# Kernel tuning notes

Measured on AMD Instinct MI355X. Metric: run time of the kernel, lower is better.

Reference implementation:

```python
import jax, jax.numpy as jnp
import numpy as np
from math import sqrt
from itertools import product

NUM_CLASSES = 21
TOP_K = 200
VAR = (0.1, 0.2)
CONF_THRESH = 0.01
NMS_THRESH = 0.45
EPS = 1e-6
BATCH = 32


def make_priors():
    # Exact SSD300 PriorBox generation (8732 boxes, cx/cy/w/h in [0,1])
    image_size = 300
    feature_maps = [38, 19, 10, 5, 3, 1]
    steps = [8, 16, 32, 64, 100, 300]
    min_sizes = [30, 60, 111, 162, 213, 264]
    max_sizes = [60, 111, 162, 213, 264, 315]
    ars = [[2], [2, 3], [2, 3], [2, 3], [2], [2]]
    mean = []
    for k, f in enumerate(feature_maps):
        for i, j in product(range(f), repeat=2):
            f_k = image_size / steps[k]
            cx = (j + 0.5) / f_k
            cy = (i + 0.5) / f_k
            s_k = min_sizes[k] / image_size
            mean += [cx, cy, s_k, s_k]
            s_kp = sqrt(s_k * (max_sizes[k] / image_size))
            mean += [cx, cy, s_kp, s_kp]
            for ar in ars[k]:
                mean += [cx, cy, s_k * sqrt(ar), s_k / sqrt(ar)]
                mean += [cx, cy, s_k / sqrt(ar), s_k * sqrt(ar)]
    pri = np.asarray(mean, np.float32).reshape(-1, 4)
    return np.clip(pri, 0.0, 1.0)


def setup_inputs() -> dict:
    key = jax.random.key(0)
    k1, k2 = jax.random.split(key)
    priors = jnp.asarray(make_priors())  # [8732, 4]
    P = priors.shape[0]
    loc = jax.random.normal(k1, (BATCH, P, 4), jnp.float32) * 0.5
    conf = jax.random.normal(k2, (BATCH, P, NUM_CLASSES), jnp.float32)
    return {"loc": loc, "conf": conf, "priors": priors}


def _decode(loc, priors):
    # calc_predicted_bboxes: cx/cy offset + clamped log-w/h, then corner clamp [0,1]
    pri = jnp.clip(priors, EPS, None)
    cx = pri[:, 0] + loc[:, 0] * VAR[0] * pri[:, 2]
    cy = pri[:, 1] + loc[:, 1] * VAR[0] * pri[:, 3]
    lw = jnp.clip(loc[:, 2] * VAR[1], -4.0, 4.0)
    lh = jnp.clip(loc[:, 3] * VAR[1], -4.0, 4.0)
    w = pri[:, 2] * jnp.exp(lw)
    h = pri[:, 3] * jnp.exp(lh)
    return jnp.stack([
        jnp.clip(cx - w / 2, 0.0, 1.0), jnp.clip(cy - h / 2, 0.0, 1.0),
        jnp.clip(cx + w / 2, 0.0, 1.0), jnp.clip(cy + h / 2, 0.0, 1.0)], axis=1)


def _iou_matrix(b):  # b: [K,4] -> [K,K]
    area = (b[:, 2] - b[:, 0]) * (b[:, 3] - b[:, 1])
    lt = jnp.maximum(b[:, None, :2], b[None, :, :2])
    rb = jnp.minimum(b[:, None, 2:], b[None, :, 2:])
    wh = jnp.clip(rb - lt, 0.0)
    inter = wh[..., 0] * wh[..., 1]
    union = area[:, None] + area[None, :] - inter
    return inter / jnp.maximum(union, 1e-12)


def _per_class(boxes, scores):
    # boxes [P,4], scores [P] -> [TOP_K, 5] rows of [score, x1, y1, x2, y2]
    valid = (scores > CONF_THRESH) \
        & (boxes[:, 2] > boxes[:, 0] + EPS) & (boxes[:, 3] > boxes[:, 1] + EPS)
    masked = jnp.where(valid, scores, -1.0)
    top_s, top_i = jax.lax.top_k(masked, TOP_K)  # highest-score candidates
    top_b = boxes[top_i]
    top_valid = top_s > CONF_THRESH  # invalid padded entries have score -1
    ious = _iou_matrix(top_b)
    pos = jnp.arange(TOP_K)

    def body(i, alive):
        keep_i = alive[i] & top_valid[i]
        suppress = keep_i & (ious[i] > NMS_THRESH) & (pos > i)
        return alive & ~suppress

    alive = jax.lax.fori_loop(0, TOP_K, body, jnp.ones(TOP_K, bool))
    keep = alive & top_valid
    # compact kept detections to the front, preserving score order
    order = jnp.argsort(jnp.where(keep, pos, TOP_K + pos))
    rows = jnp.concatenate([top_s[:, None], top_b], axis=1)[order]
    return jnp.where(keep[order][:, None], rows, 0.0)


def reference(loc, conf, priors):
    probs = jax.nn.softmax(jnp.clip(conf, -100.0, 100.0), axis=-1)  # [B,P,C]
    boxes = jax.vmap(_decode, in_axes=(0, None))(loc, priors)       # [B,P,4]

    def per_image(b, p):
        fg = jax.vmap(_per_class, in_axes=(None, 1))(b, p[:, 1:])   # [C-1,K,5]
        return jnp.concatenate([jnp.zeros((1, TOP_K, 5), b.dtype), fg], axis=0)

    return jax.vmap(per_image)(boxes, probs)  # [B, C, K, 5]
```

## Files before the change

kernel.cpp:

```cpp
#include <hip/hip_runtime.h>
#include <cstdint>

#define P_BOX 8732
#define NBOX_TOTAL 279424
#define BATCH 32
#define NCLS 21
#define NFG 20
#define TOPK 200
#define NTH 256
#define NCH 9
#define CAND_CAP 512
#define NBKT 2048
#define NORM 0xBC23D70Bu
#define LIM (1u << 26)
#define CONF_F4 1466976

typedef unsigned long long u64;

__device__ __forceinline__ uint32_t score_key(float m) {
  uint32_t b = __float_as_uint(m);
  return (b & 0x80000000u) ? ~b : (b | 0x80000000u);
}
__device__ __forceinline__ float key_score(uint32_t k) {
  uint32_t b = (k & 0x80000000u) ? (k ^ 0x80000000u) : ~k;
  return __uint_as_float(b);
}

__device__ __forceinline__ float4 decode_box(const float4 pr, const float4 lc) {
  float px = fmaxf(pr.x, 1e-6f), py = fmaxf(pr.y, 1e-6f);
  float pw = fmaxf(pr.z, 1e-6f), ph = fmaxf(pr.w, 1e-6f);
  float cx = px + lc.x * 0.1f * pw;
  float cy = py + lc.y * 0.1f * ph;
  float lw = fminf(fmaxf(lc.z * 0.2f, -4.0f), 4.0f);
  float lh = fminf(fmaxf(lc.w * 0.2f, -4.0f), 4.0f);
  float w = pw * expf(lw);
  float h = ph * expf(lh);
  float4 r;
  r.x = fminf(fmaxf(cx - 0.5f * w, 0.0f), 1.0f);
  r.y = fminf(fmaxf(cy - 0.5f * h, 0.0f), 1.0f);
  r.z = fminf(fmaxf(cx + 0.5f * w, 0.0f), 1.0f);
  r.w = fminf(fmaxf(cy + 0.5f * h, 0.0f), 1.0f);
  return r;
}

__global__ __launch_bounds__(256) void prep_kernel(
    const float* __restrict__ loc, const float* __restrict__ conf,
    const float* __restrict__ priors, uint32_t* __restrict__ keys) {
  __shared__ float s_conf[256 * 21];
  const int t = threadIdx.x;
  const int blk = blockIdx.x;
  const float4* cf4 = (const float4*)conf;
  size_t base4 = (size_t)blk * 1344;
#pragma unroll
  for (int i = t; i < 1344; i += 256) {
    size_t g4 = base4 + i;
    if (g4 < CONF_F4) ((float4*)s_conf)[i] = cf4[g4];
  }
  __syncthreads();
  int g = blk * 256 + t;
  if (g >= NBOX_TOTAL) return;
  int b = g / P_BOX, p = g - b * P_BOX;
  float x[NCLS];
  float mx = -1e30f;
#pragma unroll
  for (int i = 0; i < NCLS; ++i) {
    float v = fminf(fmaxf(s_conf[t * 21 + i], -100.0f), 100.0f);
    x[i] = v;
    mx = fmaxf(mx, v);
  }
  float s = 0.0f;
#pragma unroll
  for (int i = 0; i < NCLS; ++i) {
    x[i] = expf(x[i] - mx);
    s += x[i];
  }
  float4 bx = decode_box(((const float4*)priors)[p], ((const float4*)loc)[g]);
  bool bok = (bx.z > bx.x + 1e-6f) && (bx.w > bx.y + 1e-6f);
#pragma unroll
  for (int ci = 1; ci < NCLS; ++ci) {
    float sc = x[ci] / s;
    float m = (bok && sc > 0.01f) ? sc : -1.0f;
    keys[((size_t)(b * NFG) + (ci - 1)) * P_BOX + p] = score_key(m) - NORM;
  }
}

__device__ __forceinline__ int cnt_ge(const uint32_t* kv, uint32_t X) {
  int n = 0;
#pragma unroll
  for (int j = 0; j < NCH * 4; ++j) n += (kv[j] >= X && kv[j] < LIM) ? 1 : 0;
  return n;
}
__device__ __forceinline__ int cnt_eq_idx(const uint32_t* kv, int t, uint32_t T, uint32_t I) {
  int n = 0;
#pragma unroll
  for (int ch = 0; ch < NCH; ++ch) {
#pragma unroll
    for (int e = 0; e < 4; ++e) {
      int p = ch * 1024 + t * 4 + e;
      n += (kv[ch * 4 + e] == T && (uint32_t)(P_BOX - p) >= I) ? 1 : 0;
    }
  }
  return n;
}

__device__ __forceinline__ int block_count(int v, int t, int* s_cnt, int& it) {
#pragma unroll
  for (int o = 32; o > 0; o >>= 1) v += __shfl_down(v, o, 64);
  int slot = it % 3;
  if (t == 0) s_cnt[(it + 1) % 3] = 0;
  if ((t & 63) == 0) atomicAdd(&s_cnt[slot], v);
  __syncthreads();
  int r = s_cnt[slot];
  ++it;
  return r;
}

__device__ __forceinline__ int3 select_bucket(const int* s_hist, int* s_S,
                                              int* s_wt, int* s_res, int need,
                                              int t) {
  const int BPT = NBKT / NTH;
  int base = t * BPT;
  int ps = 0;
#pragma unroll
  for (int i = 0; i < BPT; ++i) ps += s_hist[base + i];
  int l = t & 63, w = t >> 6;
  int v = ps;
#pragma unroll
  for (int off = 1; off < 64; off <<= 1) {
    int o = __shfl_down(v, off, 64);
    v += (l + off < 64) ? o : 0;
  }
  if (l == 0) s_wt[w] = v;
  __syncthreads();
  int hi = 0;
#pragma unroll
  for (int w2 = 0; w2 < NTH / 64; ++w2) hi += (w2 > w) ? s_wt[w2] : 0;
  int S = v + hi;
  s_S[t] = S;
  __syncthreads();
  if (t == 0 && s_S[0] < need) {
    s_res[0] = 0; s_res[1] = s_S[0]; s_res[2] = 0;
  } else if (s_S[t] >= need && (t == NTH - 1 || s_S[t + 1] < need)) {
    int suf = (t == NTH - 1) ? 0 : s_S[t + 1];
    int B = base, M = 0;
    for (int j = base + BPT - 1; j >= base; --j) {
      suf += s_hist[j];
      if (suf >= need) { B = j; M = suf; break; }
    }
    s_res[0] = B; s_res[1] = M; s_res[2] = M - s_hist[B];
  }
  __syncthreads();
  return make_int3(s_res[0], s_res[1], s_res[2]);
}

template <bool USE_WS>
__global__ __launch_bounds__(256) void task_kernel(
    const float* __restrict__ loc, const float* __restrict__ conf,
    const float* __restrict__ priors, const uint32_t* __restrict__ keys,
    float* __restrict__ out) {
  const int t = threadIdx.x;
  const int task = blockIdx.x;
  const int b = task / NCLS, c = task - b * NCLS;
  float* ob = out + (size_t)task * TOPK * 5;

  if (c == 0) {
    float4 z = make_float4(0.f, 0.f, 0.f, 0.f);
    for (int i = t; i < TOPK * 5 / 4; i += NTH) ((float4*)ob)[i] = z;
    return;
  }
  const int ft = b * NFG + (c - 1);

  __shared__ alignas(16) int s_hist[NBKT];
  __shared__ alignas(16) u64 s_cand[CAND_CAP];
  __shared__ u64 s_sel[TOPK];
  __shared__ float4 s_box[TOPK];
  __shared__ float s_area[TOPK];
  __shared__ float s_score[TOPK];
  __shared__ u64 s_nxt[2][4];
  __shared__ short s_kept[TOPK];
  __shared__ int s_wt[NTH / 64];
  __shared__ int s_res[3];
  __shared__ int s_cnt[3];
  __shared__ int s_m;
  int* s_S = (int*)s_cand;
  float* s_out = (float*)s_hist;

  if (t == 0) { s_cnt[0] = 0; s_cnt[1] = 0; s_cnt[2] = 0; s_m = 0; }
  for (int i = t; i < NBKT; i += NTH) s_hist[i] = 0;

  uint32_t kv[NCH * 4];
  if (USE_WS) {
    const uint4* kp = (const uint4*)(keys + (size_t)ft * P_BOX);
#pragma unroll
    for (int ch = 0; ch < 8; ++ch) {
      uint4 v = kp[ch * 256 + t];
      kv[ch * 4 + 0] = v.x; kv[ch * 4 + 1] = v.y;
      kv[ch * 4 + 2] = v.z; kv[ch * 4 + 3] = v.w;
    }
    if (t < 135) {
      uint4 v = kp[2048 + t];
      kv[32] = v.x; kv[33] = v.y; kv[34] = v.z; kv[35] = v.w;
    } else {
      kv[32] = LIM; kv[33] = LIM; kv[34] = LIM; kv[35] = LIM;
    }
  } else {
    for (int ch = 0; ch < NCH; ++ch) {
      int p0 = ch * 1024 + 4 * t;
#pragma unroll
      for (int e = 0; e < 4; ++e) {
        int p = p0 + e;
        uint32_t k = LIM;
        if (p < P_BOX) {
          const float* cf = conf + (size_t)(b * P_BOX + p) * NCLS;
          float x[NCLS];
          float mx = -1e30f;
#pragma unroll
          for (int i = 0; i < NCLS; ++i) {
            float v = fminf(fmaxf(cf[i], -100.0f), 100.0f);
            x[i] = v;
            mx = fmaxf(mx, v);
          }
          float ssum = 0.0f, ec = 0.0f;
#pragma unroll
          for (int i = 0; i < NCLS; ++i) {
            float ex = expf(x[i] - mx);
            ssum += ex;
            if (i == c) ec = ex;
          }
          float sc = ec / ssum;
          float4 bx = decode_box(((const float4*)priors)[p],
                                 ((const float4*)loc)[(size_t)b * P_BOX + p]);
          bool valid = (sc > 0.01f) && (bx.z > bx.x + 1e-6f) && (bx.w > bx.y + 1e-6f);
          k = score_key(valid ? sc : -1.0f) - NORM;
        }
        kv[ch * 4 + e] = k;
      }
    }
  }
  __syncthreads();

#pragma unroll
  for (int j = 0; j < NCH * 4; ++j)
    if (kv[j] < LIM) atomicAdd(&s_hist[kv[j] >> 15], 1);
  __syncthreads();
  int3 r1 = select_bucket(s_hist, s_S, s_wt, s_res, TOPK, t);
  uint32_t Tp = (uint32_t)r1.x << 15;
  int M = r1.y;
  bool ex = false;
  uint32_t Tex = 0, I = 0;

  if (M > CAND_CAP) {
    uint32_t B1 = (uint32_t)r1.x;
    int above1 = r1.z;
    __syncthreads();
    for (int i = t; i < NBKT; i += NTH) s_hist[i] = 0;
    __syncthreads();
#pragma unroll
    for (int j = 0; j < NCH * 4; ++j)
      if (kv[j] < LIM && (kv[j] >> 15) == B1)
        atomicAdd(&s_hist[(kv[j] >> 4) & (NBKT - 1)], 1);
    __syncthreads();
    int3 r2 = select_bucket(s_hist, s_S, s_wt, s_res, TOPK - above1, t);
    Tp = (B1 << 15) + ((uint32_t)r2.x << 4);
    M = above1 + r2.y;
    if (M > CAND_CAP) {
      int it = 0;
      uint32_t lo = Tp, hi = LIM;
      while (hi - lo > 1) {
        uint32_t mid = lo + ((hi - lo) >> 1);
        int cnt = block_count(cnt_ge(kv, mid), t, s_cnt, it);
        if (cnt >= TOPK) lo = mid; else hi = mid;
      }
      Tex = lo;
      int G = block_count(cnt_ge(kv, Tex + 1), t, s_cnt, it);
      int R = TOPK - G;
      uint32_t lo2 = 1, hi2 = P_BOX + 1;
      while (hi2 - lo2 > 1) {
        uint32_t mid = lo2 + ((hi2 - lo2) >> 1);
        int cnt = block_count(cnt_eq_idx(kv, t, Tex, mid), t, s_cnt, it);
        if (cnt >= R) lo2 = mid; else hi2 = mid;
      }
      I = lo2;
      ex = true;
    }
  }
  __syncthreads();

  {
    const int lane = t & 63;
#pragma unroll
    for (int ch = 0; ch < NCH; ++ch) {
#pragma unroll
      for (int e = 0; e < 4; ++e) {
        uint32_t k = kv[ch * 4 + e];
        int p = ch * 1024 + 4 * t + e;
        bool take = (k < LIM) &&
                    (ex ? (k > Tex || (k == Tex && (uint32_t)(P_BOX - p) >= I))
                        : (k >= Tp));
        u64 m = __ballot(take);
        if (m) {
          int leader = __ffsll((long long)m) - 1;
          int base = 0;
          if (lane == leader) base = atomicAdd(&s_m, __popcll(m));
          base = __shfl(base, leader, 64);
          if (take) {
            int pre = __popcll(m & ((1ull << lane) - 1ull));
            int ix = base + pre;
            if (ix < CAND_CAP)
              s_cand[ix] = ((u64)k << 32) | (uint32_t)(P_BOX - p);
          }
        }
      }
    }
  }
  __syncthreads();
  M = min(s_m, CAND_CAP);
  int nsel = min(M, TOPK);

  for (int ci = t; ci < M; ci += NTH) {
    u64 mine = s_cand[ci];
    int r = 0;
    int j = 0;
    for (; j + 8 <= M; j += 8) {
      u64 a0 = s_cand[j + 0], a1 = s_cand[j + 1], a2 = s_cand[j + 2],
          a3 = s_cand[j + 3], a4 = s_cand[j + 4], a5 = s_cand[j + 5],
          a6 = s_cand[j + 6], a7 = s_cand[j + 7];
      r += (a0 > mine) + (a1 > mine) + (a2 > mine) + (a3 > mine) +
           (a4 > mine) + (a5 > mine) + (a6 > mine) + (a7 > mine);
    }
    for (; j < M; ++j) r += (s_cand[j] > mine) ? 1 : 0;
    if (r < TOPK) s_sel[r] = mine;
  }
  __syncthreads();

  if (t < TOPK) {
    if (t < nsel) {
      u64 w = s_sel[t];
      uint32_t k = (uint32_t)(w >> 32);
      int p = P_BOX - (int)(uint32_t)(w & 0xFFFFFFFFull);
      float4 bx = decode_box(((const float4*)priors)[p],
                             ((const float4*)loc)[(size_t)b * P_BOX + p]);
      s_box[t] = bx;
      s_area[t] = (bx.z - bx.x) * (bx.w - bx.y);
      s_score[t] = key_score(k + NORM);
    } else {
      s_box[t] = make_float4(0.f, 0.f, 0.f, 0.f);
      s_area[t] = 0.f;
      s_score[t] = 0.f;
    }
  }
  __syncthreads();

  float4 bj = make_float4(0.f, 0.f, 0.f, 0.f);
  float aj = 0.f;
  const bool validj = (t < nsel);
  if (validj) { bj = s_box[t]; aj = s_area[t]; }
  const int wv = t >> 6;
  u64 cm0 = 0, cm1 = 0, cm2 = 0, cm3 = 0;
#pragma unroll
  for (int band = 0; band < 4; ++band) {
    if (band > wv) break;
    const int base = band * 64;
    const int iend = min(base + 64, nsel);
    u64 w = 0;
#pragma unroll 4
    for (int i = base; i < iend; ++i) {
      float4 bi = s_box[i];
      float ai = s_area[i];
      float lx = fmaxf(bi.x, bj.x), ly = fmaxf(bi.y, bj.y);
      float rx = fminf(bi.z, bj.z), ry = fminf(bi.w, bj.w);
      float iw = fmaxf(rx - lx, 0.0f), ih = fmaxf(ry - ly, 0.0f);
      float inter = iw * ih;
      float uni = ai + aj - inter;
      float iou = inter / fmaxf(uni, 1e-12f);
      bool sup = (i < t) && validj && (iou > 0.45f);
      w |= ((u64)sup) << (i - base);
    }
    if (band == 0) cm0 = w; else if (band == 1) cm1 = w;
    else if (band == 2) cm2 = w; else cm3 = w;
  }

  int q0 = nsel, q1 = nsel - 64, q2 = nsel - 128, q3 = nsel - 192;
  u64 a0 = q0 >= 64 ? ~0ull : (q0 <= 0 ? 0ull : ((1ull << q0) - 1));
  u64 a1 = q1 >= 64 ? ~0ull : (q1 <= 0 ? 0ull : ((1ull << q1) - 1));
  u64 a2 = q2 >= 64 ? ~0ull : (q2 <= 0 ? 0ull : ((1ull << q2) - 1));
  u64 a3 = q3 >= 64 ? ~0ull : (q3 <= 0 ? 0ull : ((1ull << q3) - 1));
  for (int it2 = 0; it2 <= TOPK; ++it2) {
    bool sup = ((cm0 & a0) | (cm1 & a1) | (cm2 & a2) | (cm3 & a3)) != 0ull;
    bool na = validj && !sup;
    u64 m = __ballot(na);
    int buf = it2 & 1;
    if ((t & 63) == 0) s_nxt[buf][t >> 6] = m;
    __syncthreads();
    u64 n0 = s_nxt[buf][0], n1 = s_nxt[buf][1];
    u64 n2 = s_nxt[buf][2], n3 = s_nxt[buf][3];
    bool chg = (n0 != a0) || (n1 != a1) || (n2 != a2) || (n3 != a3);
    a0 = n0; a1 = n1; a2 = n2; a3 = n3;
    if (!chg) break;
  }

  int pc0 = __popcll(a0), pc01 = pc0 + __popcll(a1), pc012 = pc01 + __popcll(a2);
  int nk = pc012 + __popcll(a3);
  if (t < nsel) {
    int word = t >> 6, bit = t & 63;
    u64 wt = (word == 0) ? a0 : (word == 1) ? a1 : (word == 2) ? a2 : a3;
    if ((wt >> bit) & 1ull) {
      int base = (word == 0) ? 0 : (word == 1) ? pc0 : (word == 2) ? pc01 : pc012;
      int r = base + __popcll(wt & ((1ull << bit) - 1ull));
      s_kept[r] = (short)t;
    }
  }
  __syncthreads();

  if (t < TOPK) {
    float o0 = 0.f, o1 = 0.f, o2 = 0.f, o3 = 0.f, o4 = 0.f;
    if (t < nk) {
      int j = s_kept[t];
      o0 = s_score[j];
      float4 bx = s_box[j];
      o1 = bx.x; o2 = bx.y; o3 = bx.z; o4 = bx.w;
    }
    s_out[t * 5 + 0] = o0; s_out[t * 5 + 1] = o1; s_out[t * 5 + 2] = o2;
    s_out[t * 5 + 3] = o3; s_out[t * 5 + 4] = o4;
  }
  __syncthreads();
  for (int i = t; i < TOPK * 5 / 4; i += NTH)
    ((float4*)ob)[i] = ((float4*)s_out)[i];
}

extern "C" void kernel_launch(void* const* d_in, const int* in_sizes, int n_in,
                              void* d_out, int out_size, void* d_ws, size_t ws_size,
                              hipStream_t stream) {
  (void)in_sizes;
  (void)n_in;
  (void)out_size;
  const float* loc = (const float*)d_in[0];
  const float* conf = (const float*)d_in[1];
  const float* priors = (const float*)d_in[2];
  float* out = (float*)d_out;

  size_t keys_bytes = (size_t)BATCH * NFG * P_BOX * sizeof(uint32_t);
  if (ws_size >= keys_bytes) {
    uint32_t* keys = (uint32_t*)d_ws;
    int nprep = (NBOX_TOTAL + 255) / 256;
    prep_kernel<<<nprep, 256, 0, stream>>>(loc, conf, priors, keys);
    task_kernel<true><<<BATCH * NCLS, NTH, 0, stream>>>(loc, conf, priors, keys, out);
  } else {
    task_kernel<false><<<BATCH * NCLS, NTH, 0, stream>>>(loc, conf, priors, nullptr, out);
  }
}
```

Baseline: 133.2 us.

## Drop separate prep kernel and compute class scores inside each task block

Removes the prep kernel that computed softmax and box validity once per box and wrote per-class keys to workspace. Each (image, class) block now recomputes the full softmax and box decode for every prior itself. This saves a kernel launch and the write and read-back of the keys buffer. In exchange it repeats the softmax about 20 times and reads conf with strided, uncoalesced loads from every block.

Result: slower. 417.7 us (+213.5%).

```diff
diff --git a/kernel.cpp b/kernel.cpp
--- a/kernel.cpp
+++ b/kernel.cpp
@@ -2,10 +2,8 @@
 #include <cstdint>
 
 #define P_BOX 8732
-#define NBOX_TOTAL 279424
 #define BATCH 32
 #define NCLS 21
-#define NFG 20
 #define TOPK 200
 #define NTH 256
 #define NCH 9
@@ -13,7 +11,6 @@
 #define NBKT 2048
 #define NORM 0xBC23D70Bu
 #define LIM (1u << 26)
-#define CONF_F4 1466976
 
 typedef unsigned long long u64;
 
@@ -43,47 +40,6 @@
   return r;
 }
 
-__global__ __launch_bounds__(256) void prep_kernel(
-    const float* __restrict__ loc, const float* __restrict__ conf,
-    const float* __restrict__ priors, uint32_t* __restrict__ keys) {
-  __shared__ float s_conf[256 * 21];
-  const int t = threadIdx.x;
-  const int blk = blockIdx.x;
-  const float4* cf4 = (const float4*)conf;
-  size_t base4 = (size_t)blk * 1344;
-#pragma unroll
-  for (int i = t; i < 1344; i += 256) {
-    size_t g4 = base4 + i;
-    if (g4 < CONF_F4) ((float4*)s_conf)[i] = cf4[g4];
-  }
-  __syncthreads();
-  int g = blk * 256 + t;
-  if (g >= NBOX_TOTAL) return;
-  int b = g / P_BOX, p = g - b * P_BOX;
-  float x[NCLS];
-  float mx = -1e30f;
-#pragma unroll
-  for (int i = 0; i < NCLS; ++i) {
-    float v = fminf(fmaxf(s_conf[t * 21 + i], -100.0f), 100.0f);
-    x[i] = v;
-    mx = fmaxf(mx, v);
-  }
-  float s = 0.0f;
-#pragma unroll
-  for (int i = 0; i < NCLS; ++i) {
-    x[i] = expf(x[i] - mx);
-    s += x[i];
-  }
-  float4 bx = decode_box(((const float4*)priors)[p], ((const float4*)loc)[g]);
-  bool bok = (bx.z > bx.x + 1e-6f) && (bx.w > bx.y + 1e-6f);
-#pragma unroll
-  for (int ci = 1; ci < NCLS; ++ci) {
-    float sc = x[ci] / s;
-    float m = (bok && sc > 0.01f) ? sc : -1.0f;
-    keys[((size_t)(b * NFG) + (ci - 1)) * P_BOX + p] = score_key(m) - NORM;
-  }
-}
-
 __device__ __forceinline__ int cnt_ge(const uint32_t* kv, uint32_t X) {
   int n = 0;
 #pragma unroll
@@ -153,11 +109,9 @@
   return make_int3(s_res[0], s_res[1], s_res[2]);
 }
 
-template <bool USE_WS>
 __global__ __launch_bounds__(256) void task_kernel(
     const float* __restrict__ loc, const float* __restrict__ conf,
-    const float* __restrict__ priors, const uint32_t* __restrict__ keys,
-    float* __restrict__ out) {
+    const float* __restrict__ priors, float* __restrict__ out) {
   const int t = threadIdx.x;
   const int task = blockIdx.x;
   const int b = task / NCLS, c = task - b * NCLS;
@@ -168,7 +122,6 @@
     for (int i = t; i < TOPK * 5 / 4; i += NTH) ((float4*)ob)[i] = z;
     return;
   }
-  const int ft = b * NFG + (c - 1);
 
   __shared__ alignas(16) int s_hist[NBKT];
   __shared__ alignas(16) u64 s_cand[CAND_CAP];
@@ -189,52 +142,36 @@
   for (int i = t; i < NBKT; i += NTH) s_hist[i] = 0;
 
   uint32_t kv[NCH * 4];
-  if (USE_WS) {
-    const uint4* kp = (const uint4*)(keys + (size_t)ft * P_BOX);
-#pragma unroll
-    for (int ch = 0; ch < 8; ++ch) {
-      uint4 v = kp[ch * 256 + t];
-      kv[ch * 4 + 0] = v.x; kv[ch * 4 + 1] = v.y;
-      kv[ch * 4 + 2] = v.z; kv[ch * 4 + 3] = v.w;
-    }
-    if (t < 135) {
-      uint4 v = kp[2048 + t];
-      kv[32] = v.x; kv[33] = v.y; kv[34] = v.z; kv[35] = v.w;
-    } else {
-      kv[32] = LIM; kv[33] = LIM; kv[34] = LIM; kv[35] = LIM;
-    }
-  } else {
-    for (int ch = 0; ch < NCH; ++ch) {
-      int p0 = ch * 1024 + 4 * t;
-#pragma unroll
-      for (int e = 0; e < 4; ++e) {
-        int p = p0 + e;
-        uint32_t k = LIM;
-        if (p < P_BOX) {
-          const float* cf = conf + (size_t)(b * P_BOX + p) * NCLS;
-          float x[NCLS];
-          float mx = -1e30f;
-#pragma unroll
-          for (int i = 0; i < NCLS; ++i) {
-            float v = fminf(fmaxf(cf[i], -100.0f), 100.0f);
-            x[i] = v;
-            mx = fmaxf(mx, v);
-          }
-          float ssum = 0.0f, ec = 0.0f;
-#pragma unroll
-          for (int i = 0; i < NCLS; ++i) {
-            float ex = expf(x[i] - mx);
-            ssum += ex;
-            if (i == c) ec = ex;
-          }
-          float sc = ec / ssum;
-          float4 bx = decode_box(((const float4*)priors)[p],
-                                 ((const float4*)loc)[(size_t)b * P_BOX + p]);
-          bool valid = (sc > 0.01f) && (bx.z > bx.x + 1e-6f) && (bx.w > bx.y + 1e-6f);
-          k = score_key(valid ? sc : -1.0f) - NORM;
+  for (int ch = 0; ch < NCH; ++ch) {
+    int p0 = ch * 1024 + 4 * t;
+#pragma unroll
+    for (int e = 0; e < 4; ++e) {
+      int p = p0 + e;
+      uint32_t k = LIM;
+      if (p < P_BOX) {
+        const float* cf = conf + (size_t)(b * P_BOX + p) * NCLS;
+        float x[NCLS];
+        float mx = -1e30f;
+#pragma unroll
+        for (int i = 0; i < NCLS; ++i) {
+          float v = fminf(fmaxf(cf[i], -100.0f), 100.0f);
+          x[i] = v;
+          mx = fmaxf(mx, v);
         }
-        kv[ch * 4 + e] = k;
+        float ssum = 0.0f, ec = 0.0f;
+#pragma unroll
+        for (int i = 0; i < NCLS; ++i) {
+          float ex = expf(x[i] - mx);
+          ssum += ex;
+          if (i == c) ec = ex;
+        }
+        float sc = ec / ssum;
+        float4 bx = decode_box(((const float4*)priors)[p],
+                               ((const float4*)loc)[(size_t)b * P_BOX + p]);
+        bool valid = (sc > 0.01f) && (bx.z > bx.x + 1e-6f) && (bx.w > bx.y + 1e-6f);
+        k = score_key(valid ? sc : -1.0f) - NORM;
       }
+      kv[ch * 4 + e] = k;
     }
   }
   __syncthreads();
@@ -434,18 +371,12 @@
   (void)in_sizes;
   (void)n_in;
   (void)out_size;
+  (void)d_ws;
+  (void)ws_size;
   const float* loc = (const float*)d_in[0];
   const float* conf = (const float*)d_in[1];
   const float* priors = (const float*)d_in[2];
   float* out = (float*)d_out;
 
-  size_t keys_bytes = (size_t)BATCH * NFG * P_BOX * sizeof(uint32_t);
-  if (ws_size >= keys_bytes) {
-    uint32_t* keys = (uint32_t*)d_ws;
-    int nprep = (NBOX_TOTAL + 255) / 256;
-    prep_kernel<<<nprep, 256, 0, stream>>>(loc, conf, priors, keys);
-    task_kernel<true><<<BATCH * NCLS, NTH, 0, stream>>>(loc, conf, priors, keys, out);
-  } else {
-    task_kernel<false><<<BATCH * NCLS, NTH, 0, stream>>>(loc, conf, priors, nullptr, out);
-  }
-}
+  task_kernel<<<BATCH * NCLS, NTH, 0, stream>>>(loc, conf, priors, out);
+}
```
